# Optimization experiments

Measured on AMD Instinct MI355X. Metric: run time of the kernel, lower is better.

## Reference

```python
import jax, jax.numpy as jnp
import numpy as np

HEAD = 8
DIM = 512
LN_EPS = 1e-5
SCALE = (DIM / HEAD) ** (-0.5)


def _layernorm(x, g, b):
    mu = jnp.mean(x, axis=-1, keepdims=True)
    var = jnp.var(x, axis=-1, keepdims=True)
    return (x - mu) * jax.lax.rsqrt(var + LN_EPS) * g + b


def _split_heads(x):
    b, n, _ = x.shape
    return x.reshape(b, n, HEAD, DIM // HEAD).transpose(0, 2, 1, 3)  # b h n d


def _merge_heads(x):
    b, h, n, d = x.shape
    return x.transpose(0, 2, 1, 3).reshape(b, n, h * d)


def setup_inputs() -> dict:
    key = jax.random.key(0)
    ks = jax.random.split(key, 6)
    B, NI, NT = 4, 2048, 2048
    s = 0.02
    return {
        "i": jax.random.normal(ks[0], (B, NI, DIM), jnp.float32),
        "t": jax.random.normal(ks[1], (B, NT, DIM), jnp.float32),
        "g_i": jnp.ones((DIM,), jnp.float32),
        "b_i": jnp.zeros((DIM,), jnp.float32),
        "g_t": jnp.ones((DIM,), jnp.float32),
        "b_t": jnp.zeros((DIM,), jnp.float32),
        "w_qkv_i": jax.random.normal(ks[2], (DIM, 3 * DIM), jnp.float32) * s,
        "w_qkv_t": jax.random.normal(ks[3], (DIM, 3 * DIM), jnp.float32) * s,
        "w_out_i": jax.random.normal(ks[4], (DIM, DIM), jnp.float32) * s,
        "w_out_t": jax.random.normal(ks[5], (DIM, DIM), jnp.float32) * s,
    }


def reference(i, t, g_i, b_i, g_t, b_t, w_qkv_i, w_qkv_t, w_out_i, w_out_t):
    i = _layernorm(i, g_i, b_i)
    t = _layernorm(t, g_t, b_t)
    q_i, k_i, v_i = jnp.split(i @ w_qkv_i, 3, axis=-1)
    q_t, k_t, v_t = jnp.split(t @ w_qkv_t, 3, axis=-1)
    q_i, k_i, v_i = map(_split_heads, (q_i, k_i, v_i))
    q_t, k_t, v_t = map(_split_heads, (q_t, k_t, v_t))
    q_i = q_i * SCALE
    q_t = q_t * SCALE
    # i -> t cross attention (queries from image stream, keys/values from text stream)
    sim_i2t = jnp.einsum('bhid,bhjd->bhij', q_i, k_t)
    attn_i2t = jax.nn.softmax(sim_i2t, axis=-1)
    out_i2t = _merge_heads(jnp.einsum('bhij,bhjd->bhid', attn_i2t, v_t)) @ w_out_t
    # t -> i cross attention
    sim_t2i = jnp.einsum('bhid,bhjd->bhij', q_t, k_i)
    attn_t2i = jax.nn.softmax(sim_t2i, axis=-1)
    out_t2i = _merge_heads(jnp.einsum('bhij,bhjd->bhid', attn_t2i, v_i)) @ w_out_i
    return jnp.concatenate([out_t2i, out_i2t], axis=1)
```

## Files before the change

kernel.cpp:

```cpp
#include <hip/hip_runtime.h>
#include <stdint.h>

typedef short bf16x8 __attribute__((ext_vector_type(8)));
typedef float f32x4 __attribute__((ext_vector_type(4)));
typedef float f32x16 __attribute__((ext_vector_type(16)));
typedef unsigned short u16x4 __attribute__((ext_vector_type(4)));
typedef unsigned short u16x8 __attribute__((ext_vector_type(8)));
typedef unsigned int u32x4 __attribute__((ext_vector_type(4)));
typedef unsigned int u32;

#define MFMA16(a, b, c) __builtin_amdgcn_mfma_f32_16x16x32_bf16(a, b, c, 0, 0, 0)
#define MFMA32(a, b, c) __builtin_amdgcn_mfma_f32_32x32x16_bf16(a, b, c, 0, 0, 0)

static constexpr size_t LN_BYTES   = 8192ull * 512 * 2;
static constexpr size_t WQKV_BYTES = 1536ull * 512 * 2;
static constexpr size_t WOUT_BYTES = 512ull * 512 * 2;
static constexpr size_t QKV_BYTES  = 4ull * 8 * 2048 * 64 * 2;

static constexpr size_t OFF_LN0 = 0;
static constexpr size_t OFF_LN1 = OFF_LN0 + LN_BYTES;
static constexpr size_t OFF_WQ0 = OFF_LN1 + LN_BYTES;
static constexpr size_t OFF_WQ1 = OFF_WQ0 + WQKV_BYTES;
static constexpr size_t OFF_WO0 = OFF_WQ1 + WQKV_BYTES;
static constexpr size_t OFF_WO1 = OFF_WO0 + WOUT_BYTES;
static constexpr size_t OFF_Q0  = OFF_WO1 + WOUT_BYTES;
static constexpr size_t OFF_K0  = OFF_Q0 + QKV_BYTES;
static constexpr size_t OFF_VT0 = OFF_K0 + QKV_BYTES;
static constexpr size_t OFF_Q1  = OFF_VT0 + QKV_BYTES;
static constexpr size_t OFF_K1  = OFF_Q1 + QKV_BYTES;
static constexpr size_t OFF_VT1 = OFF_K1 + QKV_BYTES;
static constexpr size_t OFF_AO0 = OFF_LN0;
static constexpr size_t OFF_AO1 = OFF_LN1;

__device__ __forceinline__ unsigned short f2bf(float f) {
  union { float f; unsigned int u; } v; v.f = f;
  unsigned int r = v.u + 0x7FFFu + ((v.u >> 16) & 1u);
  return (unsigned short)(r >> 16);
}

__device__ __forceinline__ void gload16(const void* g, void* l) {
  __builtin_amdgcn_global_load_lds(
      (const __attribute__((address_space(1))) void*)g,
      (__attribute__((address_space(3))) void*)l, 16, 0, 0);
}

__device__ __forceinline__ u32 cvtpk(float lo, float hi) {
  u32 d;
  asm("v_cvt_pk_bf16_f32 %0, %1, %2" : "=v"(d) : "v"(lo), "v"(hi));
  return d;
}

__device__ __forceinline__ void plswap(u32& a, u32& b) {
  asm("v_permlane32_swap_b32 %0, %1" : "+v"(a), "+v"(b));
}

__device__ __forceinline__ f32x16 zero16() {
  f32x16 z;
#pragma unroll
  for (int i = 0; i < 16; i++) z[i] = 0.0f;
  return z;
}

__global__ __launch_bounds__(256) void wt_kernel(const float* __restrict__ w,
                                                 unsigned short* __restrict__ wt,
                                                 int K, int N) {
  __shared__ float tile[64][65];
  int n0 = blockIdx.x * 64, k0 = blockIdx.y * 64;
  int t = threadIdx.x;
  int c = t & 63, rg = t >> 6;
#pragma unroll
  for (int i = 0; i < 16; i++) {
    int kk = i * 4 + rg;
    tile[kk][c] = w[(size_t)(k0 + kk) * N + n0 + c];
  }
  __syncthreads();
#pragma unroll
  for (int i = 0; i < 16; i++) {
    int nn = i * 4 + rg;
    wt[(size_t)(n0 + nn) * K + k0 + c] = f2bf(tile[c][nn]);
  }
}

__global__ __launch_bounds__(256) void ln_kernel(
    const float* __restrict__ xi, const float* __restrict__ xt,
    const float* __restrict__ gi, const float* __restrict__ bi,
    const float* __restrict__ gt, const float* __restrict__ bt,
    char* __restrict__ ws) {
  int row = blockIdx.x * 4 + (threadIdx.x >> 6);
  int l = threadIdx.x & 63;
  const float *x, *g, *b; unsigned short* o; int r;
  if (row < 8192) { x = xi; g = gi; b = bi; o = (unsigned short*)(ws + OFF_LN0); r = row; }
  else            { x = xt; g = gt; b = bt; o = (unsigned short*)(ws + OFF_LN1); r = row - 8192; }
  const float4* xv = (const float4*)(x + (size_t)r * 512);
  float4 a0 = xv[l * 2], a1 = xv[l * 2 + 1];
  float s  = a0.x + a0.y + a0.z + a0.w + a1.x + a1.y + a1.z + a1.w;
  float ss = a0.x * a0.x + a0.y * a0.y + a0.z * a0.z + a0.w * a0.w +
             a1.x * a1.x + a1.y * a1.y + a1.z * a1.z + a1.w * a1.w;
#pragma unroll
  for (int m = 1; m < 64; m <<= 1) { s += __shfl_xor(s, m); ss += __shfl_xor(ss, m); }
  float mean = s * (1.0f / 512.0f);
  float var  = ss * (1.0f / 512.0f) - mean * mean;
  float rstd = rsqrtf(var + 1e-5f);
  const float4* gv = (const float4*)g;
  const float4* bv = (const float4*)b;
  float4 g0 = gv[l * 2], g1 = gv[l * 2 + 1], b0 = bv[l * 2], b1 = bv[l * 2 + 1];
  u16x8 ov;
  ov[0] = f2bf((a0.x - mean) * rstd * g0.x + b0.x);
  ov[1] = f2bf((a0.y - mean) * rstd * g0.y + b0.y);
  ov[2] = f2bf((a0.z - mean) * rstd * g0.z + b0.z);
  ov[3] = f2bf((a0.w - mean) * rstd * g0.w + b0.w);
  ov[4] = f2bf((a1.x - mean) * rstd * g1.x + b1.x);
  ov[5] = f2bf((a1.y - mean) * rstd * g1.y + b1.y);
  ov[6] = f2bf((a1.z - mean) * rstd * g1.z + b1.z);
  ov[7] = f2bf((a1.w - mean) * rstd * g1.w + b1.w);
  *(u16x8*)(o + (size_t)r * 512 + l * 8) = ov;
}

__device__ __forceinline__ void gemm128_core(const char* __restrict__ A,
                                             const char* __restrict__ B,
                                             int M0, int N0,
                                             char* lA, char* lB, f32x4 acc[4][4]) {
  int tid = threadIdx.x, w = tid >> 6, l = tid & 63;
  int wr = (w >> 1) * 64, wc = (w & 1) * 64;
  int l15 = l & 15, lg = l >> 4;
  int rl = l >> 3;
  int cswz = ((l & 7) ^ rl) << 4;
#pragma unroll 1
  for (int kt = 0; kt < 512; kt += 64) {
#pragma unroll
    for (int i = 0; i < 4; i++) {
      int rr = (w * 4 + i) * 8 + rl;
      gload16(A + (size_t)(M0 + rr) * 1024 + kt * 2 + cswz, lA + (w * 4 + i) * 1024);
      gload16(B + (size_t)(N0 + rr) * 1024 + kt * 2 + cswz, lB + (w * 4 + i) * 1024);
    }
    __syncthreads();
#pragma unroll
    for (int kk = 0; kk < 2; kk++) {
      bf16x8 af[4], bfv[4];
#pragma unroll
      for (int mi = 0; mi < 4; mi++) {
        int row = wr + mi * 16 + l15;
        af[mi] = *(const bf16x8*)(lA + row * 128 + ((kk * 64 + lg * 16) ^ ((row & 7) << 4)));
      }
#pragma unroll
      for (int ni = 0; ni < 4; ni++) {
        int row = wc + ni * 16 + l15;
        bfv[ni] = *(const bf16x8*)(lB + row * 128 + ((kk * 64 + lg * 16) ^ ((row & 7) << 4)));
      }
#pragma unroll
      for (int mi = 0; mi < 4; mi++)
#pragma unroll
        for (int ni = 0; ni < 4; ni++)
          acc[mi][ni] = MFMA16(af[mi], bfv[ni], acc[mi][ni]);
    }
    __syncthreads();
  }
}

__global__ __launch_bounds__(256, 2) void qkv_kernel(char* __restrict__ ws) {
  __shared__ char lA[16384];
  __shared__ char lB[16384];
  int s = blockIdx.z;
  const char* A = ws + (s ? OFF_LN1 : OFF_LN0);
  const char* B = ws + (s ? OFF_WQ1 : OFF_WQ0);
  unsigned short* qb = (unsigned short*)(ws + (s ? OFF_Q1 : OFF_Q0));
  unsigned short* kb = (unsigned short*)(ws + (s ? OFF_K1 : OFF_K0));
  unsigned short* vb = (unsigned short*)(ws + (s ? OFF_VT1 : OFF_VT0));
  int M0 = blockIdx.x * 128, N0 = blockIdx.y * 128;
  f32x4 zero = {0.f, 0.f, 0.f, 0.f};
  f32x4 acc[4][4];
#pragma unroll
  for (int mi = 0; mi < 4; mi++)
#pragma unroll
    for (int ni = 0; ni < 4; ni++) acc[mi][ni] = zero;
  gemm128_core(A, B, M0, N0, lA, lB, acc);

  int tid = threadIdx.x, w = tid >> 6, l = tid & 63;
  int wr = (w >> 1) * 64, wc = (w & 1) * 64;
  int l15 = l & 15, lg = l >> 4;
  int which = N0 >> 9;
#pragma unroll
  for (int mi = 0; mi < 4; mi++) {
    int m = M0 + wr + mi * 16 + lg * 4;
    int bb = m >> 11, t = m & 2047;
#pragma unroll
    for (int ni = 0; ni < 4; ni++) {
      int n = N0 + wc + ni * 16 + l15;
      int h = (n >> 6) & 7, d = n & 63;
      if (which == 2) {
        u16x4 pk;
        pk[0] = f2bf(acc[mi][ni][0]);
        pk[1] = f2bf(acc[mi][ni][1]);
        pk[2] = f2bf(acc[mi][ni][2]);
        pk[3] = f2bf(acc[mi][ni][3]);
        *(u16x4*)(vb + ((size_t)(bb * 8 + h) * 64 + d) * 2048 + t) = pk;
      } else {
        unsigned short* dst = (which ? kb : qb) + ((size_t)(bb * 8 + h) * 2048 + t) * 64 + d;
        float sc = which ? 1.0f : 0.125f;
#pragma unroll
        for (int r = 0; r < 4; r++) dst[(size_t)r * 64] = f2bf(acc[mi][ni][r] * sc);
      }
    }
  }
}

__global__ __launch_bounds__(256, 2) void attn_kernel(char* __restrict__ ws) {
  __shared__ char lK[2][8192];
  __shared__ char lV[2][8192];
  int dir = blockIdx.z;
  const char* kbh = ws + (dir ? OFF_K1 : OFF_K0) + (size_t)blockIdx.y * 2048 * 128;
  const char* vbh = ws + (dir ? OFF_VT1 : OFF_VT0) + (size_t)blockIdx.y * 2048 * 128;
  const char* qbh = ws + (dir ? OFF_Q0 : OFF_Q1) + (size_t)blockIdx.y * 2048 * 128;
  unsigned short* ao = (unsigned short*)(ws + (dir ? OFF_AO1 : OFF_AO0));
  int q0 = blockIdx.x * 128;

  int tid = threadIdx.x, w = tid >> 6, l = tid & 63;
  int l31 = l & 31, hi = l >> 5;
  int rl = l >> 3;
  int cswz = ((l & 7) ^ rl) << 4;
  int r7 = (l31 & 7) << 4;

  int qrow = q0 + w * 32 + l31;
  bf16x8 qf[4];
#pragma unroll
  for (int kc = 0; kc < 4; kc++)
    qf[kc] = *(const bf16x8*)(qbh + (size_t)qrow * 128 + kc * 32 + hi * 16);

  f32x16 oA = zero16(), oB = zero16();
  float mrun = -3.0e38f, lrun = 0.f;

#define STAGE(buf, kt)                                                              \
  {                                                                                 \
    _Pragma("unroll")                                                               \
    for (int i = 0; i < 2; i++) {                                                   \
      int rr = (w * 2 + i) * 8 + rl;                                                \
      gload16(kbh + (size_t)((kt) * 64 + rr) * 128 + cswz, &lK[buf][(w * 2 + i) * 1024]); \
      gload16(vbh + (size_t)rr * 4096 + (kt) * 128 + cswz, &lV[buf][(w * 2 + i) * 1024]); \
    }                                                                               \
  }

  STAGE(0, 0);
  __syncthreads();

  int cur = 0;
#pragma unroll 1
  for (int kt = 0; kt < 32; kt++) {
    if (kt < 31) STAGE(cur ^ 1, kt + 1);

    const char* K = lK[cur];
    const char* V = lV[cur];

    f32x16 sA = zero16(), sB = zero16();
    __builtin_amdgcn_s_setprio(1);
#pragma unroll
    for (int kc = 0; kc < 4; kc++) {
      bf16x8 kfA = *(const bf16x8*)(K + l31 * 128 + ((kc * 32 + hi * 16) ^ r7));
      bf16x8 kfB = *(const bf16x8*)(K + (32 + l31) * 128 + ((kc * 32 + hi * 16) ^ r7));
      sA = MFMA32(kfA, qf[kc], sA);
      sB = MFMA32(kfB, qf[kc], sB);
    }
    __builtin_amdgcn_s_setprio(0);

    float v8[8];
#pragma unroll
    for (int i = 0; i < 8; i++)
      v8[i] = fmaxf(fmaxf(sA[i], sA[i + 8]), fmaxf(sB[i], sB[i + 8]));
#pragma unroll
    for (int st = 4; st > 0; st >>= 1)
#pragma unroll
      for (int i = 0; i < 4; i++)
        if (i < st) v8[i] = fmaxf(v8[i], v8[i + st]);
    float mx = fmaxf(v8[0], __shfl_xor(v8[0], 32));
    float mn = fmaxf(mrun, mx);
    float corr = __expf(mrun - mn);
    mrun = mn;
#pragma unroll
    for (int i = 0; i < 16; i++) {
      sA[i] = __expf(sA[i] - mn);
      sB[i] = __expf(sB[i] - mn);
    }
    float s8[8];
#pragma unroll
    for (int i = 0; i < 8; i++)
      s8[i] = (sA[i] + sA[i + 8]) + (sB[i] + sB[i + 8]);
#pragma unroll
    for (int st = 4; st > 0; st >>= 1)
#pragma unroll
      for (int i = 0; i < 4; i++)
        if (i < st) s8[i] += s8[i + st];
    float rs = s8[0] + __shfl_xor(s8[0], 32);
    lrun = lrun * corr + rs;
    oA = oA * corr;
    oB = oB * corr;

#pragma unroll
    for (int kb = 0; kb < 2; kb++) {
      const f32x16& sv = kb ? sB : sA;
      u32 c0 = cvtpk(sv[0], sv[1]),   c1 = cvtpk(sv[2], sv[3]);
      u32 c2 = cvtpk(sv[4], sv[5]),   c3 = cvtpk(sv[6], sv[7]);
      u32 c4 = cvtpk(sv[8], sv[9]),   c5 = cvtpk(sv[10], sv[11]);
      u32 c6 = cvtpk(sv[12], sv[13]), c7 = cvtpk(sv[14], sv[15]);
      plswap(c0, c2); plswap(c1, c3);
      plswap(c4, c6); plswap(c5, c7);
      u32x4 p0w; p0w[0] = c0; p0w[1] = c1; p0w[2] = c2; p0w[3] = c3;
      u32x4 p1w; p1w[0] = c4; p1w[1] = c5; p1w[2] = c6; p1w[3] = c7;
      bf16x8 pf0 = __builtin_bit_cast(bf16x8, p0w);
      bf16x8 pf1 = __builtin_bit_cast(bf16x8, p1w);
      int kc0 = kb * 2, kc1 = kb * 2 + 1;
      bf16x8 vA0 = *(const bf16x8*)(V + l31 * 128 + ((kc0 * 32 + hi * 16) ^ r7));
      bf16x8 vB0 = *(const bf16x8*)(V + (32 + l31) * 128 + ((kc0 * 32 + hi * 16) ^ r7));
      bf16x8 vA1 = *(const bf16x8*)(V + l31 * 128 + ((kc1 * 32 + hi * 16) ^ r7));
      bf16x8 vB1 = *(const bf16x8*)(V + (32 + l31) * 128 + ((kc1 * 32 + hi * 16) ^ r7));
      __builtin_amdgcn_s_setprio(1);
      oA = MFMA32(vA0, pf0, oA);
      oB = MFMA32(vB0, pf0, oB);
      oA = MFMA32(vA1, pf1, oA);
      oB = MFMA32(vB1, pf1, oB);
      __builtin_amdgcn_s_setprio(0);
    }

    __syncthreads();
    cur ^= 1;
  }
#undef STAGE

  float inv = 1.0f / lrun;
  int b = blockIdx.y >> 3, h = blockIdx.y & 7;
  unsigned short* aorow = ao + ((size_t)b * 2048 + qrow) * 512 + h * 64;
#pragma unroll
  for (int g = 0; g < 4; g++) {
    u16x4 pa, pb;
#pragma unroll
    for (int j = 0; j < 4; j++) {
      pa[j] = f2bf(oA[g * 4 + j] * inv);
      pb[j] = f2bf(oB[g * 4 + j] * inv);
    }
    *(u16x4*)(aorow + g * 8 + hi * 4) = pa;
    *(u16x4*)(aorow + 32 + g * 8 + hi * 4) = pb;
  }
}

__global__ __launch_bounds__(256, 2) void proj_kernel(char* __restrict__ ws,
                                                      float* __restrict__ dout) {
  __shared__ char lA[16384];
  __shared__ char lB[16384];
  int dir = blockIdx.z;
  const char* A = ws + (dir ? OFF_AO1 : OFF_AO0);
  const char* B = ws + (dir ? OFF_WO1 : OFF_WO0);
  int M0 = blockIdx.x * 128, N0 = blockIdx.y * 128;
  f32x4 zero = {0.f, 0.f, 0.f, 0.f};
  f32x4 acc[4][4];
#pragma unroll
  for (int mi = 0; mi < 4; mi++)
#pragma unroll
    for (int ni = 0; ni < 4; ni++) acc[mi][ni] = zero;
  gemm128_core(A, B, M0, N0, lA, lB, acc);

  int tid = threadIdx.x, w = tid >> 6, l = tid & 63;
  int wr = (w >> 1) * 64, wc = (w & 1) * 64;
  int l15 = l & 15, lg = l >> 4;
#pragma unroll
  for (int mi = 0; mi < 4; mi++) {
    int m = M0 + wr + mi * 16 + lg * 4;
    int bb = m >> 11, t = m & 2047;
    size_t orow = (size_t)bb * 4096 + (size_t)dir * 2048 + t;
#pragma unroll
    for (int ni = 0; ni < 4; ni++) {
      int n = N0 + wc + ni * 16 + l15;
#pragma unroll
      for (int r = 0; r < 4; r++) dout[(orow + r) * 512 + n] = acc[mi][ni][r];
    }
  }
}

extern "C" void kernel_launch(void* const* d_in, const int* in_sizes, int n_in,
                              void* d_out, int out_size, void* d_ws, size_t ws_size,
                              hipStream_t stream) {
  const float* xi  = (const float*)d_in[0];
  const float* xt  = (const float*)d_in[1];
  const float* gi  = (const float*)d_in[2];
  const float* bi  = (const float*)d_in[3];
  const float* gt  = (const float*)d_in[4];
  const float* bt  = (const float*)d_in[5];
  const float* wqi = (const float*)d_in[6];
  const float* wqt = (const float*)d_in[7];
  const float* woi = (const float*)d_in[8];
  const float* wot = (const float*)d_in[9];
  char* ws = (char*)d_ws;
  float* out = (float*)d_out;

  wt_kernel<<<dim3(24, 8), 256, 0, stream>>>(wqi, (unsigned short*)(ws + OFF_WQ0), 512, 1536);
  wt_kernel<<<dim3(24, 8), 256, 0, stream>>>(wqt, (unsigned short*)(ws + OFF_WQ1), 512, 1536);
  wt_kernel<<<dim3(8, 8), 256, 0, stream>>>(woi, (unsigned short*)(ws + OFF_WO0), 512, 512);
  wt_kernel<<<dim3(8, 8), 256, 0, stream>>>(wot, (unsigned short*)(ws + OFF_WO1), 512, 512);
  ln_kernel<<<4096, 256, 0, stream>>>(xi, xt, gi, bi, gt, bt, ws);
  qkv_kernel<<<dim3(64, 12, 2), 256, 0, stream>>>(ws);
  attn_kernel<<<dim3(16, 32, 2), 256, 0, stream>>>(ws);
  proj_kernel<<<dim3(64, 4, 2), 256, 0, stream>>>(ws, out);
}
```

Before: 270.4 us.

## Fold log2e into Q scale, lazy rescale softmax, split tile into halves

Folds log2(e) into the Q pre-scale so the kernel can call exp2 directly. The online softmax now skips rescaling the running max and output unless the new max exceeds the old one by a threshold, and it processes the 64-key tile as two 32-key halves to lower register pressure. Launch bounds are raised to 4 blocks per CU to allow higher occupancy. The lazy rescale lets exponents grow by up to 2^11 before correction, which could affect accuracy in bf16/f32, and the higher occupancy target may force register spills.

```diff
diff --git a/kernel.cpp b/kernel.cpp
--- a/kernel.cpp
+++ b/kernel.cpp
@@ -196,7 +196,7 @@
         *(u16x4*)(vb + ((size_t)(bb * 8 + h) * 64 + d) * 2048 + t) = pk;
       } else {
         unsigned short* dst = (which ? kb : qb) + ((size_t)(bb * 8 + h) * 2048 + t) * 64 + d;
-        float sc = which ? 1.0f : 0.125f;
+        float sc = which ? 1.0f : 0.18033688011112042f;
 #pragma unroll
         for (int r = 0; r < 4; r++) dst[(size_t)r * 64] = f2bf(acc[mi][ni][r] * sc);
       }
@@ -204,7 +204,7 @@
   }
 }
 
-__global__ __launch_bounds__(256, 2) void attn_kernel(char* __restrict__ ws) {
+__global__ __launch_bounds__(256, 4) void attn_kernel(char* __restrict__ ws) {
   __shared__ char lK[2][8192];
   __shared__ char lV[2][8192];
   int dir = blockIdx.z;
@@ -250,63 +250,61 @@
     const char* K = lK[cur];
     const char* V = lV[cur];
 
-    f32x16 sA = zero16(), sB = zero16();
-    __builtin_amdgcn_s_setprio(1);
-#pragma unroll
-    for (int kc = 0; kc < 4; kc++) {
-      bf16x8 kfA = *(const bf16x8*)(K + l31 * 128 + ((kc * 32 + hi * 16) ^ r7));
-      bf16x8 kfB = *(const bf16x8*)(K + (32 + l31) * 128 + ((kc * 32 + hi * 16) ^ r7));
-      sA = MFMA32(kfA, qf[kc], sA);
-      sB = MFMA32(kfB, qf[kc], sB);
-    }
-    __builtin_amdgcn_s_setprio(0);
-
-    float v8[8];
-#pragma unroll
-    for (int i = 0; i < 8; i++)
-      v8[i] = fmaxf(fmaxf(sA[i], sA[i + 8]), fmaxf(sB[i], sB[i + 8]));
-#pragma unroll
-    for (int st = 4; st > 0; st >>= 1)
-#pragma unroll
-      for (int i = 0; i < 4; i++)
-        if (i < st) v8[i] = fmaxf(v8[i], v8[i + st]);
-    float mx = fmaxf(v8[0], __shfl_xor(v8[0], 32));
-    float mn = fmaxf(mrun, mx);
-    float corr = __expf(mrun - mn);
-    mrun = mn;
-#pragma unroll
-    for (int i = 0; i < 16; i++) {
-      sA[i] = __expf(sA[i] - mn);
-      sB[i] = __expf(sB[i] - mn);
-    }
-    float s8[8];
-#pragma unroll
-    for (int i = 0; i < 8; i++)
-      s8[i] = (sA[i] + sA[i + 8]) + (sB[i] + sB[i + 8]);
-#pragma unroll
-    for (int st = 4; st > 0; st >>= 1)
-#pragma unroll
-      for (int i = 0; i < 4; i++)
-        if (i < st) s8[i] += s8[i + st];
-    float rs = s8[0] + __shfl_xor(s8[0], 32);
-    lrun = lrun * corr + rs;
-    oA = oA * corr;
-    oB = oB * corr;
-
-#pragma unroll
-    for (int kb = 0; kb < 2; kb++) {
-      const f32x16& sv = kb ? sB : sA;
-      u32 c0 = cvtpk(sv[0], sv[1]),   c1 = cvtpk(sv[2], sv[3]);
-      u32 c2 = cvtpk(sv[4], sv[5]),   c3 = cvtpk(sv[6], sv[7]);
-      u32 c4 = cvtpk(sv[8], sv[9]),   c5 = cvtpk(sv[10], sv[11]);
-      u32 c6 = cvtpk(sv[12], sv[13]), c7 = cvtpk(sv[14], sv[15]);
+#pragma unroll
+    for (int half = 0; half < 2; half++) {
+      const char* Kh = K + half * 32 * 128;
+
+      f32x16 s = zero16();
+      __builtin_amdgcn_s_setprio(1);
+#pragma unroll
+      for (int kc = 0; kc < 4; kc++) {
+        bf16x8 kf = *(const bf16x8*)(Kh + l31 * 128 + ((kc * 32 + hi * 16) ^ r7));
+        s = MFMA32(kf, qf[kc], s);
+      }
+      __builtin_amdgcn_s_setprio(0);
+
+      float t8[8];
+#pragma unroll
+      for (int i = 0; i < 8; i++) t8[i] = fmaxf(s[i], s[i + 8]);
+#pragma unroll
+      for (int st = 4; st > 0; st >>= 1)
+#pragma unroll
+        for (int i = 0; i < 4; i++)
+          if (i < st) t8[i] = fmaxf(t8[i], t8[i + st]);
+      float mx = fmaxf(t8[0], __shfl_xor(t8[0], 32));
+
+      if (__any(mx > mrun + 11.0f)) {
+        float mn = fmaxf(mrun, mx);
+        float corr = __builtin_amdgcn_exp2f(mrun - mn);
+        mrun = mn;
+#pragma unroll
+        for (int i = 0; i < 16; i++) { oA[i] *= corr; oB[i] *= corr; }
+        lrun *= corr;
+      }
+#pragma unroll
+      for (int i = 0; i < 16; i++) s[i] = __builtin_amdgcn_exp2f(s[i] - mrun);
+
+      float u8[8];
+#pragma unroll
+      for (int i = 0; i < 8; i++) u8[i] = s[i] + s[i + 8];
+#pragma unroll
+      for (int st = 4; st > 0; st >>= 1)
+#pragma unroll
+        for (int i = 0; i < 4; i++)
+          if (i < st) u8[i] += u8[i + st];
+      lrun += u8[0] + __shfl_xor(u8[0], 32);
+
+      u32 c0 = cvtpk(s[0], s[1]),   c1 = cvtpk(s[2], s[3]);
+      u32 c2 = cvtpk(s[4], s[5]),   c3 = cvtpk(s[6], s[7]);
+      u32 c4 = cvtpk(s[8], s[9]),   c5 = cvtpk(s[10], s[11]);
+      u32 c6 = cvtpk(s[12], s[13]), c7 = cvtpk(s[14], s[15]);
       plswap(c0, c2); plswap(c1, c3);
       plswap(c4, c6); plswap(c5, c7);
       u32x4 p0w; p0w[0] = c0; p0w[1] = c1; p0w[2] = c2; p0w[3] = c3;
       u32x4 p1w; p1w[0] = c4; p1w[1] = c5; p1w[2] = c6; p1w[3] = c7;
       bf16x8 pf0 = __builtin_bit_cast(bf16x8, p0w);
       bf16x8 pf1 = __builtin_bit_cast(bf16x8, p1w);
-      int kc0 = kb * 2, kc1 = kb * 2 + 1;
+      int kc0 = half * 2, kc1 = half * 2 + 1;
       bf16x8 vA0 = *(const bf16x8*)(V + l31 * 128 + ((kc0 * 32 + hi * 16) ^ r7));
       bf16x8 vB0 = *(const bf16x8*)(V + (32 + l31) * 128 + ((kc0 * 32 + hi * 16) ^ r7));
       bf16x8 vA1 = *(const bf16x8*)(V + l31 * 128 + ((kc1 * 32 + hi * 16) ^ r7));
```

After: 265.2 us. Within noise of the previous version (-1.9%).
